# Optimization experiments

Hardware: AMD Instinct MI355X
Metric: run time of the kernel (lower is better)

The kernel has to match this reference:

```python
import jax, jax.numpy as jnp
from jax import lax
import numpy as np

B, T, F, H = 1024, 512, 64, 128


def setup_inputs() -> dict:
    key = jax.random.key(0)
    ks = jax.random.split(key, 12)
    s_in = 1.0 / np.sqrt(H)  # PyTorch LSTM init scale
    inp = {
        "x": jax.random.normal(ks[0], (B, T, F), dtype=jnp.float32),
        # layer 0 (gate order i, f, g, o as in PyTorch)
        "W_ih0": jax.random.uniform(ks[1], (4 * H, F), jnp.float32, -s_in, s_in),
        "W_hh0": jax.random.uniform(ks[2], (4 * H, H), jnp.float32, -s_in, s_in),
        "b_ih0": jax.random.uniform(ks[3], (4 * H,), jnp.float32, -s_in, s_in),
        "b_hh0": jax.random.uniform(ks[4], (4 * H,), jnp.float32, -s_in, s_in),
        # layer 1
        "W_ih1": jax.random.uniform(ks[5], (4 * H, H), jnp.float32, -s_in, s_in),
        "W_hh1": jax.random.uniform(ks[6], (4 * H, H), jnp.float32, -s_in, s_in),
        "b_ih1": jax.random.uniform(ks[7], (4 * H,), jnp.float32, -s_in, s_in),
        "b_hh1": jax.random.uniform(ks[8], (4 * H,), jnp.float32, -s_in, s_in),
        # MLP head
        "fc1_w": jax.random.uniform(ks[9], (64, H), jnp.float32, -s_in, s_in),
        "fc1_b": jnp.zeros((64,), jnp.float32),
        "fc2_w": jax.random.uniform(ks[10], (1, 64), jnp.float32, -1 / 8.0, 1 / 8.0),
        "fc2_b": jnp.zeros((1,), jnp.float32),
    }
    return inp


def _lstm_layer(x_seq, W_ih, W_hh, b_ih, b_hh):
    """x_seq: [B, T, Fin] -> hidden sequence [B, T, H]. PyTorch gate order i,f,g,o."""
    Bn = x_seq.shape[0]
    Hn = W_hh.shape[1]
    # precompute input projection for all timesteps (one big GEMM)
    x_proj = jnp.einsum("btf,gf->btg", x_seq, W_ih) + b_ih + b_hh  # [B, T, 4H]

    def step(carry, xt):
        h, c = carry
        gates = xt + h @ W_hh.T  # [B, 4H]
        i, f, g, o = jnp.split(gates, 4, axis=-1)
        i = jax.nn.sigmoid(i)
        f = jax.nn.sigmoid(f)
        g = jnp.tanh(g)
        o = jax.nn.sigmoid(o)
        c = f * c + i * g
        h = o * jnp.tanh(c)
        return (h, c), h

    h0 = jnp.zeros((Bn, Hn), x_seq.dtype)
    c0 = jnp.zeros((Bn, Hn), x_seq.dtype)
    (_, _), hs = lax.scan(step, (h0, c0), jnp.swapaxes(x_proj, 0, 1))  # hs: [T, B, H]
    return jnp.swapaxes(hs, 0, 1)


def reference(x, W_ih0, W_hh0, b_ih0, b_hh0, W_ih1, W_hh1, b_ih1, b_hh1,
              fc1_w, fc1_b, fc2_w, fc2_b):
    h1 = _lstm_layer(x, W_ih0, W_hh0, b_ih0, b_hh0)   # [B, T, H]
    h2 = _lstm_layer(h1, W_ih1, W_hh1, b_ih1, b_hh1)  # [B, T, H]
    last = h2[:, -1, :]                                # [B, H]
    out = jax.nn.relu(last @ fc1_w.T + fc1_b)          # [B, 64]
    out = out @ fc2_w.T + fc2_b                        # [B, 1]
    return out
```

## Files before the change

### kernel.cpp

```cpp
#include <hip/hip_runtime.h>
#include <math.h>


#define BB 1024
#define TT 512
#define FF 64
#define HH 128
#define LOG2E 1.44269504088896340736f
#define TWOLOG2E 2.88539008177792681472f

typedef __attribute__((ext_vector_type(8))) short     v8s;
typedef __attribute__((ext_vector_type(8))) _Float16  v8h;
typedef __attribute__((ext_vector_type(4))) float     v4f;

__device__ __forceinline__ short bf16r(float v) {
    unsigned u = __float_as_uint(v);
    return (short)((u + 0x7FFFu + ((u >> 16) & 1u)) >> 16);
}
__device__ __forceinline__ float bf16tof(short s) {
    return __uint_as_float(((unsigned)(unsigned short)s) << 16);
}
__device__ __forceinline__ float rcp1p(float y) {
    return __builtin_amdgcn_rcpf(1.0f + __builtin_exp2f(y));
}
__device__ __forceinline__ void light_barrier() {
    asm volatile("s_waitcnt lgkmcnt(0)\n\ts_barrier" ::: "memory");
}
__device__ __forceinline__ void heavy_barrier() {
    asm volatile("s_waitcnt vmcnt(0) lgkmcnt(0)\n\ts_barrier" ::: "memory");
}
__device__ __forceinline__ void wait_flag_ge(int* f, int need) {
    for (int i = 0; i < 2000000; ++i) {
        int v = __hip_atomic_fetch_add(f, 0, __ATOMIC_ACQUIRE,
                                       __HIP_MEMORY_SCOPE_AGENT);
        if (v >= need) return;
        __builtin_amdgcn_s_sleep(4);
    }
}
__device__ __forceinline__ void split2(float a, float b,
                                       unsigned& hi, unsigned& lo) {
    unsigned ua = __float_as_uint(a), ub = __float_as_uint(b);
    hi = (ua >> 16) | (ub & 0xFFFF0000u);
    float ra = a - __uint_as_float(ua & 0xFFFF0000u);
    float rb = b - __uint_as_float(ub & 0xFFFF0000u);
    lo = (__float_as_uint(ra) >> 16) | (__float_as_uint(rb) & 0xFFFF0000u);
}


#define REC_STEP(CUR, NXT, tv, STORE_HS)                                       \
  {                                                                            \
    v4f g0 = *(const v4f*)&xbuf[CUR][(0 * 128 + jh) * 20 + quad * 4];          \
    v4f g1 = *(const v4f*)&xbuf[CUR][(1 * 128 + jh) * 20 + quad * 4];          \
    v4f g2 = *(const v4f*)&xbuf[CUR][(2 * 128 + jh) * 20 + quad * 4];          \
    v4f g3 = *(const v4f*)&xbuf[CUR][(3 * 128 + jh) * 20 + quad * 4];          \
    v8h ah[4];                                                                 \
    _Pragma("unroll") for (int q = 0; q < 4; ++q)                              \
        ah[q] = *(const v8h*)&hbuf[CUR][lane16 * 136 + q * 32 + quad * 8];     \
    _Pragma("unroll") for (int q = 0; q < 4; ++q) {                            \
      g0 = __builtin_amdgcn_mfma_f32_16x16x32_f16(ah[q], bh[0][q], g0, 0, 0, 0);\
      g1 = __builtin_amdgcn_mfma_f32_16x16x32_f16(ah[q], bh[1][q], g1, 0, 0, 0);\
      g2 = __builtin_amdgcn_mfma_f32_16x16x32_f16(ah[q], bh[2][q], g2, 0, 0, 0);\
      g3 = __builtin_amdgcn_mfma_f32_16x16x32_f16(ah[q], bh[3][q], g3, 0, 0, 0);\
    }                                                                          \
    _Pragma("unroll") for (int r = 0; r < 4; ++r) {                            \
      float ig = rcp1p(-g0[r]);                                                \
      float fg = rcp1p(-g1[r]);                                                \
      float gt = fmaf(-2.0f, rcp1p(g2[r]), 1.0f);                              \
      float og = rcp1p(-g3[r]);                                                \
      c[r] = fmaf(fg, c[r], ig * gt);                                          \
      float th = fmaf(-2.0f, rcp1p(TWOLOG2E * c[r]), 1.0f);                    \
      float h = og * th;                                                       \
      hbuf[NXT][(quad * 4 + r) * 136 + jh] = (_Float16)h;                      \
      if ((STORE_HS) && (tv) == TT - 1)                                        \
        hs[(b0 + quad * 4 + r) * HH + jh] = h;                                 \
    }                                                                          \
  }

#define PHELP_STEP(CUR, NXT, tv)                                               \
  {                                                                            \
    float2 xnew = *(const float2*)xp;                                          \
    if ((tv) < TT - 4) xp += FF;                                               \
    if ((tv) > 0) {                                                            \
      uint2 hv = *(const uint2*)&hbuf[CUR][hr_row * 136 + hr_col];             \
      *(uint2*)hcs = hv;                                                       \
      hcs += (long)BB * HH;                                                    \
    }                                                                          \
    v8s xh[2], xl[2];                                                          \
    _Pragma("unroll") for (int q = 0; q < 2; ++q) {                            \
      xh[q] = *(const v8s*)&pool[NXT][0][lane16 * 72 + q * 32 + quad * 8];     \
      xl[q] = *(const v8s*)&pool[NXT][1][lane16 * 72 + q * 32 + quad * 8];     \
    }                                                                          \
    _Pragma("unroll") for (int g = 0; g < 4; ++g) {                            \
      v4f a = {bias[g], bias[g], bias[g], bias[g]};                            \
      a = __builtin_amdgcn_mfma_f32_16x16x32_bf16(xh[0], bxh[g][0], a, 0, 0, 0);\
      a = __builtin_amdgcn_mfma_f32_16x16x32_bf16(xh[0], bxl[g][0], a, 0, 0, 0);\
      a = __builtin_amdgcn_mfma_f32_16x16x32_bf16(xl[0], bxh[g][0], a, 0, 0, 0);\
      a = __builtin_amdgcn_mfma_f32_16x16x32_bf16(xh[1], bxh[g][1], a, 0, 0, 0);\
      a = __builtin_amdgcn_mfma_f32_16x16x32_bf16(xh[1], bxl[g][1], a, 0, 0, 0);\
      a = __builtin_amdgcn_mfma_f32_16x16x32_bf16(xl[1], bxh[g][1], a, 0, 0, 0);\
      *(v4f*)&xbuf[NXT][(g * 128 + jh) * 20 + quad * 4] = a;                   \
    }                                                                          \
    {                                                                          \
      unsigned hi_, lo_;                                                       \
      split2(xreg.x, xreg.y, hi_, lo_);                                        \
      *(unsigned*)&pool[CUR][0][xr_row * 72 + xr_col] = hi_;                   \
      *(unsigned*)&pool[CUR][1][xr_row * 72 + xr_col] = lo_;                   \
    }                                                                          \
    xreg = xnew;                                                               \
  }

#define CHELP_STEP(CUR, NXT, tv)                                               \
  {                                                                            \
    v8h a1[4];                                                                 \
    _Pragma("unroll") for (int q = 0; q < 4; ++q)                              \
        a1[q] = *(const v8h*)&sb[(NXT) * 2176 + lane16 * 136 + q * 32 + quad * 8];\
    _Pragma("unroll") for (int g = 0; g < 4; ++g) {                            \
      v4f a = {bias[g], bias[g], bias[g], bias[g]};                            \
      _Pragma("unroll") for (int q = 0; q < 4; ++q)                            \
          a = __builtin_amdgcn_mfma_f32_16x16x32_f16(a1[q], bi[g][q], a, 0, 0, 0);\
      *(v4f*)&xbuf[NXT][(g * 128 + jh) * 20 + quad * 4] = a;                   \
    }                                                                          \
    *(uint2*)&sb[(CUR) * 2176 + hr_row * 136 + hr_col] = hreg;                 \
    hreg = *(const uint2*)hp;                                                  \
    if ((tv) < TT - 4) hp += (long)BB * HH;                                    \
  }

__global__ __launch_bounds__(1024, 1) void fused_lstm_kernel(
    const float* __restrict__ x,
    const float* __restrict__ Wih0, const float* __restrict__ Whh0,
    const float* __restrict__ bih0, const float* __restrict__ bhh0,
    const float* __restrict__ Wih1, const float* __restrict__ Whh1,
    const float* __restrict__ bih1, const float* __restrict__ bhh1,
    _Float16* __restrict__ h1c, float* __restrict__ hs, int* __restrict__ flags)
{
    const int tid = threadIdx.x;
    const bool isrec = tid < 512;
    const int l = tid & 63;
    const int lane16 = l & 15;
    const int quad = l >> 4;
    const int jh = 16 * ((tid >> 6) & 7) + lane16;
    const int stid = tid & 511;
    const int hr_row = stid >> 5;
    const int hr_col = (stid & 31) * 4;

    __shared__ __align__(16) _Float16 hbuf[2][16 * 136];
    __shared__ __align__(16) short    pool[2][2][16 * 72];
    __shared__ __align__(16) float    xbuf[2][512 * 20];

    if (blockIdx.x < 64) {
        const int tile = blockIdx.x;
        const long b0 = (long)tile * 16;
        int* flagp = &flags[tile];

        if (isrec) {
            v8h bh[4][4];
#pragma unroll
            for (int g = 0; g < 4; ++g) {
                const int col = g * 128 + jh;
                const float sg = (g == 2) ? TWOLOG2E : LOG2E;
#pragma unroll
                for (int q = 0; q < 4; ++q) {
                    const float* p = &Whh0[(long)col * HH + q * 32 + quad * 8];
                    float4 u0 = *(const float4*)p;
                    float4 u1 = *(const float4*)(p + 4);
                    v8h t;
                    t[0]=(_Float16)(u0.x*sg); t[1]=(_Float16)(u0.y*sg);
                    t[2]=(_Float16)(u0.z*sg); t[3]=(_Float16)(u0.w*sg);
                    t[4]=(_Float16)(u1.x*sg); t[5]=(_Float16)(u1.y*sg);
                    t[6]=(_Float16)(u1.z*sg); t[7]=(_Float16)(u1.w*sg);
                    bh[g][q] = t;
                }
            }
            for (int i = tid; i < 16 * 136; i += 512) hbuf[0][i] = (_Float16)0.0f;
            float c[4] = {0.f, 0.f, 0.f, 0.f};
            __syncthreads();
            light_barrier();

            for (int tp = 0; tp < TT / 2; ++tp) {
                REC_STEP(0, 1, 2 * tp, 0);
                light_barrier();
                REC_STEP(1, 0, 2 * tp + 1, 0);
                light_barrier();
                if ((tp & 3) == 3 && tid == 0)
                    __hip_atomic_store(flagp, 2 * tp + 1, __ATOMIC_RELEASE,
                                       __HIP_MEMORY_SCOPE_AGENT);
            }
            light_barrier();
            if (tid == 0)
                __hip_atomic_store(flagp, TT, __ATOMIC_RELEASE,
                                   __HIP_MEMORY_SCOPE_AGENT);
        } else {
            float bias[4];
            v8s bxh[4][2], bxl[4][2];
#pragma unroll
            for (int g = 0; g < 4; ++g) {
                const int col = g * 128 + jh;
                const float sg = (g == 2) ? TWOLOG2E : LOG2E;
                bias[g] = (bih0[col] + bhh0[col]) * sg;
#pragma unroll
                for (int q = 0; q < 2; ++q) {
                    const float* p = &Wih0[(long)col * FF + q * 32 + quad * 8];
                    float4 u0 = *(const float4*)p;
                    float4 u1 = *(const float4*)(p + 4);
                    float vv[8] = {u0.x,u0.y,u0.z,u0.w,u1.x,u1.y,u1.z,u1.w};
                    v8s hi, lo;
#pragma unroll
                    for (int e = 0; e < 8; ++e) {
                        float vs = vv[e] * sg;
                        short hbits = bf16r(vs);
                        hi[e] = hbits;
                        lo[e] = bf16r(vs - bf16tof(hbits));
                    }
                    bxh[g][q] = hi; bxl[g][q] = lo;
                }
            }
            const int xr_row = stid >> 5;
            const int xr_col = (stid & 31) * 2;
            const float* xp = &x[(b0 + xr_row) * TT * FF + xr_col];
            float2 x0v  = *(const float2*)xp;
            float2 x1v  = *(const float2*)(xp + FF);
            float2 xreg = *(const float2*)(xp + 2 * FF);
            xp += 3 * FF;
            {
                unsigned hi, lo; split2(x0v.x, x0v.y, hi, lo);
                *(unsigned*)&pool[0][0][xr_row * 72 + xr_col] = hi;
                *(unsigned*)&pool[0][1][xr_row * 72 + xr_col] = lo;
            }
            __syncthreads();
            {
                v8s xh[2], xl[2];
#pragma unroll
                for (int q = 0; q < 2; ++q) {
                    xh[q] = *(const v8s*)&pool[0][0][lane16 * 72 + q * 32 + quad * 8];
                    xl[q] = *(const v8s*)&pool[0][1][lane16 * 72 + q * 32 + quad * 8];
                }
#pragma unroll
                for (int g = 0; g < 4; ++g) {
                    v4f a = {bias[g], bias[g], bias[g], bias[g]};
                    a = __builtin_amdgcn_mfma_f32_16x16x32_bf16(xh[0], bxh[g][0], a, 0, 0, 0);
                    a = __builtin_amdgcn_mfma_f32_16x16x32_bf16(xh[0], bxl[g][0], a, 0, 0, 0);
                    a = __builtin_amdgcn_mfma_f32_16x16x32_bf16(xl[0], bxh[g][0], a, 0, 0, 0);
                    a = __builtin_amdgcn_mfma_f32_16x16x32_bf16(xh[1], bxh[g][1], a, 0, 0, 0);
                    a = __builtin_amdgcn_mfma_f32_16x16x32_bf16(xh[1], bxl[g][1], a, 0, 0, 0);
                    a = __builtin_amdgcn_mfma_f32_16x16x32_bf16(xl[1], bxh[g][1], a, 0, 0, 0);
                    *(v4f*)&xbuf[0][(g * 128 + jh) * 20 + quad * 4] = a;
                }
            }
            {
                unsigned hi, lo; split2(x1v.x, x1v.y, hi, lo);
                *(unsigned*)&pool[1][0][xr_row * 72 + xr_col] = hi;
                *(unsigned*)&pool[1][1][xr_row * 72 + xr_col] = lo;
            }
            light_barrier();

            _Float16* hcs = h1c + (b0 + hr_row) * HH + hr_col;
            for (int tp = 0; tp < TT / 2; ++tp) {
                PHELP_STEP(0, 1, 2 * tp);
                light_barrier();
                PHELP_STEP(1, 0, 2 * tp + 1);
                if ((tp & 3) == 3) heavy_barrier();
                else               light_barrier();
            }
            {
                uint2 hv = *(const uint2*)&hbuf[0][hr_row * 136 + hr_col];
                *(uint2*)hcs = hv;
            }
            heavy_barrier();
        }
    } else {
        const int tile = blockIdx.x - 64;
        const long b0 = (long)tile * 16;
        int* flagp = &flags[tile];
        _Float16* sb = (_Float16*)&pool[0][0][0];

        if (isrec) {
            v8h bh[4][4];
#pragma unroll
            for (int g = 0; g < 4; ++g) {
                const int col = g * 128 + jh;
                const float sg = (g == 2) ? TWOLOG2E : LOG2E;
#pragma unroll
                for (int q = 0; q < 4; ++q) {
                    const float* ph = &Whh1[(long)col * HH + q * 32 + quad * 8];
                    float4 v0 = *(const float4*)ph;
                    float4 v1 = *(const float4*)(ph + 4);
                    v8h s;
                    s[0]=(_Float16)(v0.x*sg); s[1]=(_Float16)(v0.y*sg);
                    s[2]=(_Float16)(v0.z*sg); s[3]=(_Float16)(v0.w*sg);
                    s[4]=(_Float16)(v1.x*sg); s[5]=(_Float16)(v1.y*sg);
                    s[6]=(_Float16)(v1.z*sg); s[7]=(_Float16)(v1.w*sg);
                    bh[g][q] = s;
                }
            }
            for (int i = tid; i < 16 * 136; i += 512) hbuf[0][i] = (_Float16)0.0f;
            float c[4] = {0.f, 0.f, 0.f, 0.f};
            if (tid == 0) wait_flag_ge(flagp, 15);
            __syncthreads();
            light_barrier();
            light_barrier();

            for (int tp = 0; tp < TT / 2; ++tp) {
                if ((tp & 3) == 0 && tp > 0) {
                    if (tid == 0)
                        wait_flag_ge(flagp, (2 * tp + 15 < TT) ? 2 * tp + 15 : TT);
                    light_barrier();
                }
                REC_STEP(0, 1, 2 * tp, 1);
                light_barrier();
                REC_STEP(1, 0, 2 * tp + 1, 1);
                light_barrier();
            }
        } else {
            float bias[4];
            v8h bi[4][4];
#pragma unroll
            for (int g = 0; g < 4; ++g) {
                const int col = g * 128 + jh;
                const float sg = (g == 2) ? TWOLOG2E : LOG2E;
                bias[g] = (bih1[col] + bhh1[col]) * sg;
#pragma unroll
                for (int q = 0; q < 4; ++q) {
                    const float* pi = &Wih1[(long)col * HH + q * 32 + quad * 8];
                    float4 u0 = *(const float4*)pi;
                    float4 u1 = *(const float4*)(pi + 4);
                    v8h t;
                    t[0]=(_Float16)(u0.x*sg); t[1]=(_Float16)(u0.y*sg);
                    t[2]=(_Float16)(u0.z*sg); t[3]=(_Float16)(u0.w*sg);
                    t[4]=(_Float16)(u1.x*sg); t[5]=(_Float16)(u1.y*sg);
                    t[6]=(_Float16)(u1.z*sg); t[7]=(_Float16)(u1.w*sg);
                    bi[g][q] = t;
                }
            }
            __syncthreads();

            const _Float16* hp = h1c + (b0 + hr_row) * HH + hr_col;
            uint2 h0v  = *(const uint2*)hp;
            uint2 h1v  = *(const uint2*)(hp + (long)BB * HH);
            uint2 hreg = *(const uint2*)(hp + 2L * BB * HH);
            hp += 3L * BB * HH;
            *(uint2*)&sb[0 * 2176 + hr_row * 136 + hr_col] = h0v;
            light_barrier();
            {
                v8h a1[4];
#pragma unroll
                for (int q = 0; q < 4; ++q)
                    a1[q] = *(const v8h*)&sb[0 * 2176 + lane16 * 136 + q * 32 + quad * 8];
#pragma unroll
                for (int g = 0; g < 4; ++g) {
                    v4f a = {bias[g], bias[g], bias[g], bias[g]};
#pragma unroll
                    for (int q = 0; q < 4; ++q)
                        a = __builtin_amdgcn_mfma_f32_16x16x32_f16(a1[q], bi[g][q], a, 0, 0, 0);
                    *(v4f*)&xbuf[0][(g * 128 + jh) * 20 + quad * 4] = a;
                }
            }
            *(uint2*)&sb[1 * 2176 + hr_row * 136 + hr_col] = h1v;
            light_barrier();

            for (int tp = 0; tp < TT / 2; ++tp) {
                if ((tp & 3) == 0 && tp > 0) light_barrier();
                CHELP_STEP(0, 1, 2 * tp);
                light_barrier();
                CHELP_STEP(1, 0, 2 * tp + 1);
                light_barrier();
            }
        }
    }
}

__global__ __launch_bounds__(64) void head_kernel(
    const float* __restrict__ h, const float* __restrict__ w1,
    const float* __restrict__ b1, const float* __restrict__ w2,
    const float* __restrict__ b2, float* __restrict__ out)
{
    const int b = blockIdx.x;
    const int n = threadIdx.x;
    float acc = b1[n];
#pragma unroll
    for (int k = 0; k < HH; ++k)
        acc = fmaf(w1[n * HH + k], h[b * HH + k], acc);
    float v = fmaxf(acc, 0.0f) * w2[n];
#pragma unroll
    for (int off = 32; off > 0; off >>= 1)
        v += __shfl_down(v, off);
    if (n == 0) out[b] = v + b2[0];
}

extern "C" void kernel_launch(void* const* d_in, const int* in_sizes, int n_in,
                              void* d_out, int out_size, void* d_ws, size_t ws_size,
                              hipStream_t stream)
{
    const float* x    = (const float*)d_in[0];
    const float* Wih0 = (const float*)d_in[1];
    const float* Whh0 = (const float*)d_in[2];
    const float* bih0 = (const float*)d_in[3];
    const float* bhh0 = (const float*)d_in[4];
    const float* Wih1 = (const float*)d_in[5];
    const float* Whh1 = (const float*)d_in[6];
    const float* bih1 = (const float*)d_in[7];
    const float* bhh1 = (const float*)d_in[8];
    const float* w1   = (const float*)d_in[9];
    const float* b1   = (const float*)d_in[10];
    const float* w2   = (const float*)d_in[11];
    const float* b2   = (const float*)d_in[12];
    float* out = (float*)d_out;

    char* ws = (char*)d_ws;
    _Float16* h1c = (_Float16*)ws;
    float* hs  = (float*)(ws + (size_t)BB * TT * HH * sizeof(_Float16));
    int* flags = (int*)(ws + (size_t)BB * TT * HH * sizeof(_Float16)
                           + (size_t)BB * HH * sizeof(float));

    hipMemsetAsync(flags, 0, 64 * sizeof(int), stream);

    fused_lstm_kernel<<<128, 1024, 0, stream>>>(
        x, Wih0, Whh0, bih0, bhh0, Wih1, Whh1, bih1, bhh1, h1c, hs, flags);
    head_kernel<<<BB, 64, 0, stream>>>(hs, w1, b1, w2, b2, out);
}
```

Measured before the change: 873.6 us.

## Triple-buffer input projections and load MFMA fragments directly from global memory

Replaces the double-buffered xbuf with a three-slot ring so helper waves can write projections a step further ahead. The recurrent waves prefetch their gate preactivations into registers right after the nonlinearity, taking the LDS read off the critical path. Helper waves now load x and h1 fragments straight from global memory into MFMA operand registers, dropping the LDS staging pool and its split/store round trip. The cost is more LDS for the third slot, strided global fragment loads, and a more delicate producer/consumer barrier protocol.

```diff
diff --git a/kernel.cpp b/kernel.cpp
--- a/kernel.cpp
+++ b/kernel.cpp
@@ -8,6 +8,7 @@
 #define HH 128
 #define LOG2E 1.44269504088896340736f
 #define TWOLOG2E 2.88539008177792681472f
+#define XSLOT (512 * 20)
 
 typedef __attribute__((ext_vector_type(8))) short     v8s;
 typedef __attribute__((ext_vector_type(8))) _Float16  v8h;
@@ -45,17 +46,23 @@
     float rb = b - __uint_as_float(ub & 0xFFFF0000u);
     lo = (__float_as_uint(ra) >> 16) | (__float_as_uint(rb) & 0xFFFF0000u);
 }
+__device__ __forceinline__ void mk_frag(const float4& a, const float4& b,
+                                        v8s& hi, v8s& lo) {
+    unsigned h0,l0,h1,l1,h2,l2,h3,l3;
+    split2(a.x, a.y, h0, l0); split2(a.z, a.w, h1, l1);
+    split2(b.x, b.y, h2, l2); split2(b.z, b.w, h3, l3);
+    unsigned* H = (unsigned*)&hi; unsigned* L = (unsigned*)&lo;
+    H[0]=h0; H[1]=h1; H[2]=h2; H[3]=h3;
+    L[0]=l0; L[1]=l1; L[2]=l2; L[3]=l3;
+}
 
 
 #define REC_STEP(CUR, NXT, tv, STORE_HS)                                       \
   {                                                                            \
-    v4f g0 = *(const v4f*)&xbuf[CUR][(0 * 128 + jh) * 20 + quad * 4];          \
-    v4f g1 = *(const v4f*)&xbuf[CUR][(1 * 128 + jh) * 20 + quad * 4];          \
-    v4f g2 = *(const v4f*)&xbuf[CUR][(2 * 128 + jh) * 20 + quad * 4];          \
-    v4f g3 = *(const v4f*)&xbuf[CUR][(3 * 128 + jh) * 20 + quad * 4];          \
     v8h ah[4];                                                                 \
     _Pragma("unroll") for (int q = 0; q < 4; ++q)                              \
         ah[q] = *(const v8h*)&hbuf[CUR][lane16 * 136 + q * 32 + quad * 8];     \
+    v4f g0 = xacc[0], g1 = xacc[1], g2 = xacc[2], g3 = xacc[3];                \
     _Pragma("unroll") for (int q = 0; q < 4; ++q) {                            \
       g0 = __builtin_amdgcn_mfma_f32_16x16x32_f16(ah[q], bh[0][q], g0, 0, 0, 0);\
       g1 = __builtin_amdgcn_mfma_f32_16x16x32_f16(ah[q], bh[1][q], g1, 0, 0, 0);\
@@ -74,55 +81,56 @@
       if ((STORE_HS) && (tv) == TT - 1)                                        \
         hs[(b0 + quad * 4 + r) * HH + jh] = h;                                 \
     }                                                                          \
+    _Pragma("unroll") for (int g = 0; g < 4; ++g)                              \
+        xacc[g] = *(const v4f*)&xb[sA + g * 2560 + jh * 20 + quad * 4];        \
+    sA = (sA == 2 * XSLOT) ? 0 : sA + XSLOT;                                   \
+    light_barrier();                                                           \
   }
 
-#define PHELP_STEP(CUR, NXT, tv)                                               \
+#define PHELP_STEP(CUR, tv, HEAVY)                                             \
   {                                                                            \
-    float2 xnew = *(const float2*)xp;                                          \
-    if ((tv) < TT - 4) xp += FF;                                               \
     if ((tv) > 0) {                                                            \
       uint2 hv = *(const uint2*)&hbuf[CUR][hr_row * 136 + hr_col];             \
       *(uint2*)hcs = hv;                                                       \
       hcs += (long)BB * HH;                                                    \
     }                                                                          \
-    v8s xh[2], xl[2];                                                          \
-    _Pragma("unroll") for (int q = 0; q < 2; ++q) {                            \
-      xh[q] = *(const v8s*)&pool[NXT][0][lane16 * 72 + q * 32 + quad * 8];     \
-      xl[q] = *(const v8s*)&pool[NXT][1][lane16 * 72 + q * 32 + quad * 8];     \
+    v8s xh0, xl0, xh1, xl1;                                                    \
+    mk_frag(pf0, pf1, xh0, xl0);                                               \
+    mk_frag(pf2, pf3, xh1, xl1);                                               \
+    {                                                                          \
+      const float* p_ = xrow + (long)((tv) + 3 < TT ? (tv) + 3 : TT - 1) * FF; \
+      pf0 = *(const float4*)p_;        pf1 = *(const float4*)(p_ + 4);         \
+      pf2 = *(const float4*)(p_ + 32); pf3 = *(const float4*)(p_ + 36);        \
     }                                                                          \
     _Pragma("unroll") for (int g = 0; g < 4; ++g) {                            \
       v4f a = {bias[g], bias[g], bias[g], bias[g]};                            \
-      a = __builtin_amdgcn_mfma_f32_16x16x32_bf16(xh[0], bxh[g][0], a, 0, 0, 0);\
-      a = __builtin_amdgcn_mfma_f32_16x16x32_bf16(xh[0], bxl[g][0], a, 0, 0, 0);\
-      a = __builtin_amdgcn_mfma_f32_16x16x32_bf16(xl[0], bxh[g][0], a, 0, 0, 0);\
-      a = __builtin_amdgcn_mfma_f32_16x16x32_bf16(xh[1], bxh[g][1], a, 0, 0, 0);\
-      a = __builtin_amdgcn_mfma_f32_16x16x32_bf16(xh[1], bxl[g][1], a, 0, 0, 0);\
-      a = __builtin_amdgcn_mfma_f32_16x16x32_bf16(xl[1], bxh[g][1], a, 0, 0, 0);\
-      *(v4f*)&xbuf[NXT][(g * 128 + jh) * 20 + quad * 4] = a;                   \
-    }                                                                          \
-    {                                                                          \
-      unsigned hi_, lo_;                                                       \
-      split2(xreg.x, xreg.y, hi_, lo_);                                        \
-      *(unsigned*)&pool[CUR][0][xr_row * 72 + xr_col] = hi_;                   \
-      *(unsigned*)&pool[CUR][1][xr_row * 72 + xr_col] = lo_;                   \
-    }                                                                          \
-    xreg = xnew;                                                               \
+      a = __builtin_amdgcn_mfma_f32_16x16x32_bf16(xh0, bxh[g][0], a, 0, 0, 0); \
+      a = __builtin_amdgcn_mfma_f32_16x16x32_bf16(xh0, bxl[g][0], a, 0, 0, 0); \
+      a = __builtin_amdgcn_mfma_f32_16x16x32_bf16(xl0, bxh[g][0], a, 0, 0, 0); \
+      a = __builtin_amdgcn_mfma_f32_16x16x32_bf16(xh1, bxh[g][1], a, 0, 0, 0); \
+      a = __builtin_amdgcn_mfma_f32_16x16x32_bf16(xh1, bxl[g][1], a, 0, 0, 0); \
+      a = __builtin_amdgcn_mfma_f32_16x16x32_bf16(xl1, bxh[g][1], a, 0, 0, 0); \
+      *(v4f*)&xb[sW + g * 2560 + jh * 20 + quad * 4] = a;                      \
+    }                                                                          \
+    sW = (sW == 2 * XSLOT) ? 0 : sW + XSLOT;                                   \
+    if (HEAVY) heavy_barrier(); else light_barrier();                          \
   }
 
-#define CHELP_STEP(CUR, NXT, tv)                                               \
+#define CHELP_STEP(tv)                                                         \
   {                                                                            \
-    v8h a1[4];                                                                 \
-    _Pragma("unroll") for (int q = 0; q < 4; ++q)                              \
-        a1[q] = *(const v8h*)&sb[(NXT) * 2176 + lane16 * 136 + q * 32 + quad * 8];\
     _Pragma("unroll") for (int g = 0; g < 4; ++g) {                            \
       v4f a = {bias[g], bias[g], bias[g], bias[g]};                            \
       _Pragma("unroll") for (int q = 0; q < 4; ++q)                            \
-          a = __builtin_amdgcn_mfma_f32_16x16x32_f16(a1[q], bi[g][q], a, 0, 0, 0);\
-      *(v4f*)&xbuf[NXT][(g * 128 + jh) * 20 + quad * 4] = a;                   \
-    }                                                                          \
-    *(uint2*)&sb[(CUR) * 2176 + hr_row * 136 + hr_col] = hreg;                 \
-    hreg = *(const uint2*)hp;                                                  \
-    if ((tv) < TT - 4) hp += (long)BB * HH;                                    \
+          a = __builtin_amdgcn_mfma_f32_16x16x32_f16(a1n[q], bi[g][q], a, 0, 0, 0);\
+      *(v4f*)&xb[sW + g * 2560 + jh * 20 + quad * 4] = a;                      \
+    }                                                                          \
+    {                                                                          \
+      const _Float16* p_ = hrow + (long)((tv)+3 < TT ? (tv)+3 : TT-1) * BB * HH;\
+      _Pragma("unroll") for (int q = 0; q < 4; ++q)                            \
+          a1n[q] = *(const v8h*)(p_ + 32 * q);                                 \
+    }                                                                          \
+    sW = (sW == 2 * XSLOT) ? 0 : sW + XSLOT;                                   \
+    light_barrier();                                                           \
   }
 
 __global__ __launch_bounds__(1024, 1) void fused_lstm_kernel(
@@ -144,8 +152,7 @@
     const int hr_col = (stid & 31) * 4;
 
     __shared__ __align__(16) _Float16 hbuf[2][16 * 136];
-    __shared__ __align__(16) short    pool[2][2][16 * 72];
-    __shared__ __align__(16) float    xbuf[2][512 * 20];
+    __shared__ __align__(16) float    xb[3 * XSLOT];
 
     if (blockIdx.x < 64) {
         const int tile = blockIdx.x;
@@ -174,13 +181,16 @@
             for (int i = tid; i < 16 * 136; i += 512) hbuf[0][i] = (_Float16)0.0f;
             float c[4] = {0.f, 0.f, 0.f, 0.f};
             __syncthreads();
-            light_barrier();
+
+            v4f xacc[4];
+#pragma unroll
+            for (int g = 0; g < 4; ++g)
+                xacc[g] = *(const v4f*)&xb[0 + g * 2560 + jh * 20 + quad * 4];
+            int sA = XSLOT;
 
             for (int tp = 0; tp < TT / 2; ++tp) {
                 REC_STEP(0, 1, 2 * tp, 0);
-                light_barrier();
                 REC_STEP(1, 0, 2 * tp + 1, 0);
-                light_barrier();
                 if ((tp & 3) == 3 && tid == 0)
                     __hip_atomic_store(flagp, 2 * tp + 1, __ATOMIC_RELEASE,
                                        __HIP_MEMORY_SCOPE_AGENT);
@@ -214,52 +224,52 @@
                     bxh[g][q] = hi; bxl[g][q] = lo;
                 }
             }
-            const int xr_row = stid >> 5;
-            const int xr_col = (stid & 31) * 2;
-            const float* xp = &x[(b0 + xr_row) * TT * FF + xr_col];
-            float2 x0v  = *(const float2*)xp;
-            float2 x1v  = *(const float2*)(xp + FF);
-            float2 xreg = *(const float2*)(xp + 2 * FF);
-            xp += 3 * FF;
+            const float* xrow = x + (b0 + lane16) * (long)TT * FF + quad * 8;
+            float4 pf0, pf1, pf2, pf3;
             {
-                unsigned hi, lo; split2(x0v.x, x0v.y, hi, lo);
-                *(unsigned*)&pool[0][0][xr_row * 72 + xr_col] = hi;
-                *(unsigned*)&pool[0][1][xr_row * 72 + xr_col] = lo;
-            }
-            __syncthreads();
-            {
-                v8s xh[2], xl[2];
-#pragma unroll
-                for (int q = 0; q < 2; ++q) {
-                    xh[q] = *(const v8s*)&pool[0][0][lane16 * 72 + q * 32 + quad * 8];
-                    xl[q] = *(const v8s*)&pool[0][1][lane16 * 72 + q * 32 + quad * 8];
-                }
+                float4 a0 = *(const float4*)xrow;
+                float4 a1 = *(const float4*)(xrow + 4);
+                float4 a2 = *(const float4*)(xrow + 32);
+                float4 a3 = *(const float4*)(xrow + 36);
+                v8s xh0, xl0, xh1, xl1;
+                mk_frag(a0, a1, xh0, xl0); mk_frag(a2, a3, xh1, xl1);
 #pragma unroll
                 for (int g = 0; g < 4; ++g) {
                     v4f a = {bias[g], bias[g], bias[g], bias[g]};
-                    a = __builtin_amdgcn_mfma_f32_16x16x32_bf16(xh[0], bxh[g][0], a, 0, 0, 0);
-                    a = __builtin_amdgcn_mfma_f32_16x16x32_bf16(xh[0], bxl[g][0], a, 0, 0, 0);
-                    a = __builtin_amdgcn_mfma_f32_16x16x32_bf16(xl[0], bxh[g][0], a, 0, 0, 0);
-                    a = __builtin_amdgcn_mfma_f32_16x16x32_bf16(xh[1], bxh[g][1], a, 0, 0, 0);
-                    a = __builtin_amdgcn_mfma_f32_16x16x32_bf16(xh[1], bxl[g][1], a, 0, 0, 0);
-                    a = __builtin_amdgcn_mfma_f32_16x16x32_bf16(xl[1], bxh[g][1], a, 0, 0, 0);
-                    *(v4f*)&xbuf[0][(g * 128 + jh) * 20 + quad * 4] = a;
-                }
-            }
-            {
-                unsigned hi, lo; split2(x1v.x, x1v.y, hi, lo);
-                *(unsigned*)&pool[1][0][xr_row * 72 + xr_col] = hi;
-                *(unsigned*)&pool[1][1][xr_row * 72 + xr_col] = lo;
-            }
-            light_barrier();
-
+                    a = __builtin_amdgcn_mfma_f32_16x16x32_bf16(xh0, bxh[g][0], a, 0, 0, 0);
+                    a = __builtin_amdgcn_mfma_f32_16x16x32_bf16(xh0, bxl[g][0], a, 0, 0, 0);
+                    a = __builtin_amdgcn_mfma_f32_16x16x32_bf16(xl0, bxh[g][0], a, 0, 0, 0);
+                    a = __builtin_amdgcn_mfma_f32_16x16x32_bf16(xh1, bxh[g][1], a, 0, 0, 0);
+                    a = __builtin_amdgcn_mfma_f32_16x16x32_bf16(xh1, bxl[g][1], a, 0, 0, 0);
+                    a = __builtin_amdgcn_mfma_f32_16x16x32_bf16(xl1, bxh[g][1], a, 0, 0, 0);
+                    *(v4f*)&xb[0 + g * 2560 + jh * 20 + quad * 4] = a;
+                }
+                const float* p1 = xrow + FF;
+                a0 = *(const float4*)p1;        a1 = *(const float4*)(p1 + 4);
+                a2 = *(const float4*)(p1 + 32); a3 = *(const float4*)(p1 + 36);
+                mk_frag(a0, a1, xh0, xl0); mk_frag(a2, a3, xh1, xl1);
+#pragma unroll
+                for (int g = 0; g < 4; ++g) {
+                    v4f a = {bias[g], bias[g], bias[g], bias[g]};
+                    a = __builtin_amdgcn_mfma_f32_16x16x32_bf16(xh0, bxh[g][0], a, 0, 0, 0);
+                    a = __builtin_amdgcn_mfma_f32_16x16x32_bf16(xh0, bxl[g][0], a, 0, 0, 0);
+                    a = __builtin_amdgcn_mfma_f32_16x16x32_bf16(xl0, bxh[g][0], a, 0, 0, 0);
+                    a = __builtin_amdgcn_mfma_f32_16x16x32_bf16(xh1, bxh[g][1], a, 0, 0, 0);
+                    a = __builtin_amdgcn_mfma_f32_16x16x32_bf16(xh1, bxl[g][1], a, 0, 0, 0);
+                    a = __builtin_amdgcn_mfma_f32_16x16x32_bf16(xl1, bxh[g][1], a, 0, 0, 0);
+                    *(v4f*)&xb[XSLOT + g * 2560 + jh * 20 + quad * 4] = a;
+                }
+                const float* p2 = xrow + 2 * FF;
+                pf0 = *(const float4*)p2;        pf1 = *(const float4*)(p2 + 4);
+                pf2 = *(const float4*)(p2 + 32); pf3 = *(const float4*)(p2 + 36);
+            }
+            __syncthreads();
+            int sW = 2 * XSLOT;
             _Float16* hcs = h1c + (b0 + hr_row) * HH + hr_col;
+
             for (int tp = 0; tp < TT / 2; ++tp) {
-                PHELP_STEP(0, 1, 2 * tp);
-                light_barrier();
-                PHELP_STEP(1, 0, 2 * tp + 1);
-                if ((tp & 3) == 3) heavy_barrier();
-                else               light_barrier();
+                PHELP_STEP(0, 2 * tp, 0);
+                PHELP_STEP(1, 2 * tp + 1, ((tp & 3) == 3));
             }
             {
                 uint2 hv = *(const uint2*)&hbuf[0][hr_row * 136 + hr_col];
@@ -271,7 +281,6 @@
         const int tile = blockIdx.x - 64;
         const long b0 = (long)tile * 16;
         int* flagp = &flags[tile];
-        _Float16* sb = (_Float16*)&pool[0][0][0];
 
         if (isrec) {
             v8h bh[4][4];
@@ -297,7 +306,12 @@
             if (tid == 0) wait_flag_ge(flagp, 15);
             __syncthreads();
             light_barrier();
-            light_barrier();
+
+            v4f xacc[4];
+#pragma unroll
+            for (int g = 0; g < 4; ++g)
+                xacc[g] = *(const v4f*)&xb[0 + g * 2560 + jh * 20 + quad * 4];
+            int sA = XSLOT;
 
             for (int tp = 0; tp < TT / 2; ++tp) {
                 if ((tp & 3) == 0 && tp > 0) {
@@ -306,9 +320,7 @@
                     light_barrier();
                 }
                 REC_STEP(0, 1, 2 * tp, 1);
-                light_barrier();
                 REC_STEP(1, 0, 2 * tp + 1, 1);
-                light_barrier();
             }
         } else {
             float bias[4];
@@ -331,38 +343,45 @@
                     bi[g][q] = t;
                 }
             }
+            const _Float16* hrow = h1c + (b0 + lane16) * HH + quad * 8;
             __syncthreads();
 
-            const _Float16* hp = h1c + (b0 + hr_row) * HH + hr_col;
-            uint2 h0v  = *(const uint2*)hp;
-            uint2 h1v  = *(const uint2*)(hp + (long)BB * HH);
-            uint2 hreg = *(const uint2*)(hp + 2L * BB * HH);
-            hp += 3L * BB * HH;
-            *(uint2*)&sb[0 * 2176 + hr_row * 136 + hr_col] = h0v;
-            light_barrier();
+            v8h a1n[4];
             {
-                v8h a1[4];
+                v8h t0[4];
 #pragma unroll
                 for (int q = 0; q < 4; ++q)
-                    a1[q] = *(const v8h*)&sb[0 * 2176 + lane16 * 136 + q * 32 + quad * 8];
+                    t0[q] = *(const v8h*)(hrow + 32 * q);
 #pragma unroll
                 for (int g = 0; g < 4; ++g) {
                     v4f a = {bias[g], bias[g], bias[g], bias[g]};
 #pragma unroll
                     for (int q = 0; q < 4; ++q)
-                        a = __builtin_amdgcn_mfma_f32_16x16x32_f16(a1[q], bi[g][q], a, 0, 0, 0);
-                    *(v4f*)&xbuf[0][(g * 128 + jh) * 20 + quad * 4] = a;
-                }
-            }
-            *(uint2*)&sb[1 * 2176 + hr_row * 136 + hr_col] = h1v;
+                        a = __builtin_amdgcn_mfma_f32_16x16x32_f16(t0[q], bi[g][q], a, 0, 0, 0);
+                    *(v4f*)&xb[0 + g * 2560 + jh * 20 + quad * 4] = a;
+                }
+#pragma unroll
+                for (int q = 0; q < 4; ++q)
+                    t0[q] = *(const v8h*)(hrow + (long)BB * HH + 32 * q);
+#pragma unroll
+                for (int g = 0; g < 4; ++g) {
+                    v4f a = {bias[g], bias[g], bias[g], bias[g]};
+#pragma unroll
+                    for (int q = 0; q < 4; ++q)
+                        a = __builtin_amdgcn_mfma_f32_16x16x32_f16(t0[q], bi[g][q], a, 0, 0, 0);
+                    *(v4f*)&xb[XSLOT + g * 2560 + jh * 20 + quad * 4] = a;
+                }
+#pragma unroll
+                for (int q = 0; q < 4; ++q)
+                    a1n[q] = *(const v8h*)(hrow + 2L * BB * HH + 32 * q);
+            }
             light_barrier();
+            int sW = 2 * XSLOT;
 
             for (int tp = 0; tp < TT / 2; ++tp) {
                 if ((tp & 3) == 0 && tp > 0) light_barrier();
-                CHELP_STEP(0, 1, 2 * tp);
-                light_barrier();
-                CHELP_STEP(1, 0, 2 * tp + 1);
-                light_barrier();
+                CHELP_STEP(2 * tp);
+                CHELP_STEP(2 * tp + 1);
             }
         }
     }
```

After: 1.315 ms. 1.51x slower.
